# Optimization experiments

Measured on AMD Instinct MI355X. Metric: run time of the kernel, lower is better.

The kernel has to match this reference:

```python
import jax, jax.numpy as jnp
import numpy as np

D_MODEL, HEADS, GROUPS, DIM_HEAD = 256, 8, 8, 64
INNER = HEADS * DIM_HEAD              # 512
OFF_DIMS = INNER // GROUPS            # 64 channels fed to the offset network per group
DF, OFF_SCALE, KS, PAD = 4, 4.0, 6, 1  # downsample_factor, offset_scale, kernel, (6-4)//2
CPB_DIM = D_MODEL // 4                # 64
NUM_LAYERS = 6
SCALE = DIM_HEAD ** -0.5
B, H, W = 1, 40, 40


def grouped_conv1x1(x, w, g):
    # x: (b, cin, h, w); w: (cout, cin//g) torch grouped 1x1 conv weight (squeezed)
    b, cin, h, wd = x.shape
    cout = w.shape[0]
    xg = x.reshape(b, g, cin // g, h, wd)
    wg = w.reshape(g, cout // g, cin // g)
    return jnp.einsum('goi,bgihw->bgohw', wg, xg).reshape(b, cout, h, wd)


def create_grid(h, w, dtype):
    # torch meshgrid(arange(w), arange(h), indexing='xy') stacked at dim 0
    ys, xs = jnp.meshgrid(jnp.arange(h, dtype=dtype), jnp.arange(w, dtype=dtype), indexing='ij')
    return jnp.stack((xs, ys))  # (2, h, w): channel0 = x, channel1 = y


def normalize_grid(grid):
    # faithful to source: channel0 scaled by (h-1), channel1 by (w-1); out dim last
    h, w = grid.shape[-2:]
    g0 = 2.0 * grid[..., 0, :, :] / max(h - 1, 1) - 1.0
    g1 = 2.0 * grid[..., 1, :, :] / max(w - 1, 1) - 1.0
    return jnp.stack((g0, g1), axis=-1)


def grid_sample_bilinear(img, grid):
    # torch F.grid_sample, mode='bilinear', padding_mode='zeros', align_corners=False
    Bn, C, Hh, Ww = img.shape
    gx = ((grid[..., 0] + 1.0) * Ww - 1.0) * 0.5
    gy = ((grid[..., 1] + 1.0) * Hh - 1.0) * 0.5
    x0 = jnp.floor(gx)
    y0 = jnp.floor(gy)
    wx1 = gx - x0
    wy1 = gy - y0
    flat = img.reshape(Bn, C, Hh * Ww)

    def gather(xi, yi):
        valid = (xi >= 0) & (xi <= Ww - 1) & (yi >= 0) & (yi <= Hh - 1)
        xc = jnp.clip(xi, 0, Ww - 1).astype(jnp.int32)
        yc = jnp.clip(yi, 0, Hh - 1).astype(jnp.int32)
        idx = (yc * Ww + xc).reshape(Bn, 1, -1)
        vals = jnp.take_along_axis(flat, idx, axis=2).reshape(Bn, C, *xi.shape[1:])
        return vals * valid[:, None].astype(img.dtype)

    return (gather(x0, y0) * ((1 - wx1) * (1 - wy1))[:, None]
            + gather(x0 + 1, y0) * (wx1 * (1 - wy1))[:, None]
            + gather(x0, y0 + 1) * ((1 - wx1) * wy1)[:, None]
            + gather(x0 + 1, y0 + 1) * (wx1 * wy1)[:, None])


def deform_attn(x, wq, wk, wv, w_off1, b_off1, w_off2,
                cpb_w0, cpb_b0, cpb_w1, cpb_b1, cpb_w2, cpb_b2, w_out, b_out):
    b, c, Hh, Ww = x.shape
    bg = b * GROUPS
    q = grouped_conv1x1(x, wq, GROUPS)                      # (b, 512, H, W)
    qg = q.reshape(bg, OFF_DIMS, Hh, Ww)                    # group heads: (b g) d h w
    # offset network: depthwise 6x6 stride-4 conv -> GELU -> 1x1 -> tanh * scale
    off = jax.lax.conv_general_dilated(
        qg, w_off1, (DF, DF), ((PAD, PAD), (PAD, PAD)),
        dimension_numbers=('NCHW', 'OIHW', 'NCHW'), feature_group_count=OFF_DIMS)
    off = jax.nn.gelu(off + b_off1[None, :, None, None], approximate=False)
    off = jnp.tanh(jnp.einsum('oc,bchw->bohw', w_off2, off)) * OFF_SCALE  # (bg,2,h',w')
    hp, wp = off.shape[-2:]
    vgrid = create_grid(hp, wp, x.dtype)[None] + off
    vgrid_scaled = normalize_grid(vgrid)                    # (bg, h', w', 2)
    xg = x.reshape(bg, c // GROUPS, Hh, Ww)
    kv = grid_sample_bilinear(xg, vgrid_scaled).reshape(b, c, hp, wp)
    k = grouped_conv1x1(kv, wk, GROUPS)
    v = grouped_conv1x1(kv, wv, GROUPS)
    i, j = Hh * Ww, hp * wp
    qh = (q * SCALE).reshape(b, HEADS, DIM_HEAD, i).transpose(0, 1, 3, 2)  # bhid
    kh = k.reshape(b, HEADS, DIM_HEAD, j).transpose(0, 1, 3, 2)
    vh = v.reshape(b, HEADS, DIM_HEAD, j).transpose(0, 1, 3, 2)
    sim = jnp.einsum('bhid,bhjd->bhij', qh, kh)
    # continuous positional bias (CPB, depth-2 MLP on signed-log relative coords)
    grid_q = normalize_grid(create_grid(Hh, Ww, x.dtype)).reshape(i, 2)
    grid_kv = vgrid_scaled.reshape(bg, j, 2)
    pos = grid_q[None, :, None, :] - grid_kv[:, None, :, :]  # (bg, i, j, 2)
    bias = jnp.sign(pos) * jnp.log1p(jnp.abs(pos))
    bias = jax.nn.relu(bias @ cpb_w0.T + cpb_b0)
    bias = jax.nn.relu(bias @ cpb_w1.T + cpb_b1)
    bias = bias @ cpb_w2.T + cpb_b2                          # (bg, i, j, 1)
    sim = sim + bias.reshape(b, GROUPS, i, j)                # heads//offset_groups == 1
    attn = jax.nn.softmax(sim, axis=-1)                      # stable softmax (matches amax-subtract)
    out = jnp.einsum('bhij,bhjd->bhid', attn, vh)
    out = out.transpose(0, 1, 3, 2).reshape(b, INNER, Hh, Ww)
    return jnp.einsum('oc,bchw->bohw', w_out, out) + b_out[None, :, None, None]


def setup_inputs() -> dict:
    key = jax.random.key(0)
    ks = jax.random.split(key, 16)
    L = NUM_LAYERS

    def p(k, shape, scale=0.02):
        return jax.random.normal(k, shape, dtype=jnp.float32) * scale

    return {
        'bev_feat': jax.random.normal(ks[0], (B, D_MODEL, H, W), dtype=jnp.float32),
        'wq': p(ks[1], (L, INNER, D_MODEL // GROUPS)),
        'wk': p(ks[2], (L, INNER, D_MODEL // GROUPS)),
        'wv': p(ks[3], (L, INNER, D_MODEL // GROUPS)),
        'w_off1': p(ks[4], (L, OFF_DIMS, 1, KS, KS)),
        'b_off1': jnp.zeros((L, OFF_DIMS), jnp.float32),
        'w_off2': p(ks[5], (L, 2, OFF_DIMS)),
        'cpb_w0': p(ks[6], (L, CPB_DIM, 2), 0.5),
        'cpb_b0': jnp.zeros((L, CPB_DIM), jnp.float32),
        'cpb_w1': p(ks[7], (L, CPB_DIM, CPB_DIM), 0.1),
        'cpb_b1': jnp.zeros((L, CPB_DIM), jnp.float32),
        'cpb_w2': p(ks[8], (L, 1, CPB_DIM), 0.1),
        'cpb_b2': jnp.zeros((L, 1), jnp.float32),
        'w_out': p(ks[9], (L, D_MODEL, INNER)),
        'b_out': jnp.zeros((L, D_MODEL), jnp.float32),
    }


def reference(bev_feat, wq, wk, wv, w_off1, b_off1, w_off2,
              cpb_w0, cpb_b0, cpb_w1, cpb_b1, cpb_w2, cpb_b2, w_out, b_out):
    # The source encoder loop runs `output = layer(bev_feat)` on the ORIGINAL
    # input each iteration, so only the last layer's output survives. Faithful
    # math = apply layer NUM_LAYERS-1 once (dropout in eval mode -> identity).
    l = NUM_LAYERS - 1
    return deform_attn(bev_feat, wq[l], wk[l], wv[l], w_off1[l], b_off1[l], w_off2[l],
                       cpb_w0[l], cpb_b0[l], cpb_w1[l], cpb_b1[l], cpb_w2[l], cpb_b2[l],
                       w_out[l], b_out[l])
```

## Files before the change

### kernel.cpp

```cpp
#include <hip/hip_runtime.h>
#include <math.h>


#define NP 1600
#define NJ 100

typedef _Float16 f16x8 __attribute__((ext_vector_type(8)));
typedef float  f32x4  __attribute__((ext_vector_type(4)));
typedef float  f32x2  __attribute__((ext_vector_type(2)));

template<int CTRL>
__device__ __forceinline__ float dpp_add(float x) {
  int y = __builtin_amdgcn_update_dpp(0, __builtin_bit_cast(int, x),
                                      CTRL, 0xf, 0xf, true);
  return x + __builtin_bit_cast(float, y);
}

__global__ __launch_bounds__(256) void k_conv1x1(
    const float* __restrict__ x, const float* __restrict__ w,
    float* __restrict__ out, float* __restrict__ out_t) {
  int b = blockIdx.x;
  int g = b / 40;
  int r = b - g * 40;
  int oc = r / 5;
  int p0 = (r - oc * 5) * 320;
  int co0 = g * 64 + oc * 8;
  const float* xg = x + g * 32 * NP;
  const float* wr = w + co0 * 32;
  for (int p = p0 + threadIdx.x; p < p0 + 320; p += 256) {
    float acc[8];
#pragma unroll
    for (int o = 0; o < 8; ++o) acc[o] = 0.f;
#pragma unroll
    for (int ci = 0; ci < 32; ++ci) {
      float xv = xg[ci * NP + p];
#pragma unroll
      for (int o = 0; o < 8; ++o) acc[o] = fmaf(wr[o * 32 + ci], xv, acc[o]);
    }
#pragma unroll
    for (int o = 0; o < 8; ++o) out[(co0 + o) * NP + p] = acc[o];
    f32x4 t0, t1;
    t0[0] = acc[0]; t0[1] = acc[1]; t0[2] = acc[2]; t0[3] = acc[3];
    t1[0] = acc[4]; t1[1] = acc[5]; t1[2] = acc[6]; t1[3] = acc[7];
    *(f32x4*)(out_t + (size_t)p * 512 + co0) = t0;
    *(f32x4*)(out_t + (size_t)p * 512 + co0 + 4) = t1;
  }
}

__global__ __launch_bounds__(256, 4) void k_off_cpb(
    const float* __restrict__ qt, const float* __restrict__ wdw,
    const float* __restrict__ bdw, const float* __restrict__ wo2,
    const float* __restrict__ x, const float* __restrict__ wk,
    const float* __restrict__ wv,
    const float* __restrict__ w0, const float* __restrict__ b0,
    const float* __restrict__ w1, const float* __restrict__ b1v,
    const float* __restrict__ cw2, const float* __restrict__ b2,
    float* __restrict__ kout, float* __restrict__ vout_t,
    float* __restrict__ bias_t) {
  __shared__ float psum[4][72];
  __shared__ float su_l[40];
  __shared__ float sv_l[40];
  __shared__ _Float16 a16[40][72];
  __shared__ _Float16 c16[40][72];
  int gj = blockIdx.x;
  int g = gj / 100;
  int j = gj - g * 100;
  int t = threadIdx.x;
  int lane = t & 63;
  int wv_id = t >> 6;
  int oy = j / 10, ox = j - (j / 10) * 10;

  {
    float acc = 0.f;
    const float* qrow = qt + g * 64 + lane;
#pragma unroll
    for (int tu = 0; tu < 9; ++tu) {
      int tt = wv_id * 9 + tu;
      int ky = tt / 6, kx = tt - (tt / 6) * 6;
      int iy = oy * 4 - 1 + ky;
      int ix = ox * 4 - 1 + kx;
      if (iy >= 0 && iy < 40 && ix >= 0 && ix < 40)
        acc = fmaf(wdw[lane * 36 + tt], qrow[(size_t)(iy * 40 + ix) * 512], acc);
    }
    psum[wv_id][lane] = acc;
  }
  __syncthreads();

  if (wv_id == 0) {
    float accd = psum[0][lane] + psum[1][lane] + psum[2][lane] + psum[3][lane]
               + bdw[lane];
    float od = 0.5f * accd * (1.0f + erff(accd * 0.70710678118654752440f));
    float px = wo2[lane] * od, py = wo2[64 + lane] * od;
#pragma unroll
    for (int m = 1; m < 64; m <<= 1) {
      px += __shfl_xor(px, m);
      py += __shfl_xor(py, m);
    }
    float ax = tanhf(px) * 4.f;
    float ay = tanhf(py) * 4.f;
    float vx = (float)ox + ax;
    float vy = (float)oy + ay;
    float g0 = 2.f * vx / 9.f - 1.f;
    float g1 = 2.f * vy / 9.f - 1.f;
    if (lane < 40) {
      float qc = (float)lane * (2.f / 39.f) - 1.f;
      float u = qc - g0;
      float vv2 = qc - g1;
      su_l[lane] = copysignf(log1pf(fabsf(u)), u);
      sv_l[lane] = copysignf(log1pf(fabsf(vv2)), vv2);
    }
    float gx = ((g0 + 1.f) * 40.f - 1.f) * 0.5f;
    float gy = ((g1 + 1.f) * 40.f - 1.f) * 0.5f;
    float x0f = floorf(gx), y0f = floorf(gy);
    float wx = gx - x0f, wy = gy - y0f;
    bool mx0 = (x0f >= 0.f) && (x0f <= 39.f);
    bool mx1 = (x0f + 1.f >= 0.f) && (x0f + 1.f <= 39.f);
    bool my0 = (y0f >= 0.f) && (y0f <= 39.f);
    bool my1 = (y0f + 1.f >= 0.f) && (y0f + 1.f <= 39.f);
    int ix0 = (int)fminf(fmaxf(x0f, 0.f), 39.f);
    int ix1 = (int)fminf(fmaxf(x0f + 1.f, 0.f), 39.f);
    int iy0 = (int)fminf(fmaxf(y0f, 0.f), 39.f);
    int iy1 = (int)fminf(fmaxf(y0f + 1.f, 0.f), 39.f);
    float w00 = (1.f - wx) * (1.f - wy) * ((mx0 && my0) ? 1.f : 0.f);
    float w10 = wx * (1.f - wy) * ((mx1 && my0) ? 1.f : 0.f);
    float w01 = (1.f - wx) * wy * ((mx0 && my1) ? 1.f : 0.f);
    float w11 = wx * wy * ((mx1 && my1) ? 1.f : 0.f);
    int b00 = iy0 * 40 + ix0, b10 = iy0 * 40 + ix1;
    int b01 = iy1 * 40 + ix0, b11 = iy1 * 40 + ix1;
    float kvc = 0.f;
    if (lane < 32) {
      const float* xc = x + (g * 32 + lane) * NP;
      kvc = w00 * xc[b00] + w10 * xc[b10] + w01 * xc[b01] + w11 * xc[b11];
    }
    const float* wkr = wk + (g * 64 + lane) * 32;
    const float* wvr = wv + (g * 64 + lane) * 32;
    float wkreg[32], wvreg[32];
#pragma unroll
    for (int q4 = 0; q4 < 8; ++q4) {
      f32x4 a = *(const f32x4*)(wkr + q4 * 4);
      f32x4 bq = *(const f32x4*)(wvr + q4 * 4);
#pragma unroll
      for (int e = 0; e < 4; ++e) { wkreg[q4 * 4 + e] = a[e]; wvreg[q4 * 4 + e] = bq[e]; }
    }
    float kacc = 0.f, vacc = 0.f;
#pragma unroll
    for (int c = 0; c < 32; ++c) {
      float kvb = __shfl(kvc, c);
      kacc = fmaf(wkreg[c], kvb, kacc);
      vacc = fmaf(wvreg[c], kvb, vacc);
    }
    kout[(g * 64 + lane) * 100 + j] = kacc;
    vout_t[(size_t)gj * 64 + lane] = vacc;
  }
  __syncthreads();

  for (int idx = t; idx < 2560; idx += 256) {
    int xi = idx >> 6, kk = idx & 63;
    a16[xi][kk] = (_Float16)fmaf(w0[2 * kk], su_l[xi], b0[kk]);
    c16[xi][kk] = (_Float16)(w0[2 * kk + 1] * sv_l[xi]);
  }

  int row = lane & 15;
  int kgrp = lane >> 4;
  f16x8 B[4][2];
#pragma unroll
  for (int ct = 0; ct < 4; ++ct)
#pragma unroll
    for (int s = 0; s < 2; ++s)
#pragma unroll
      for (int e = 0; e < 8; ++e)
        B[ct][s][e] = (_Float16)w1[(ct * 16 + row) * 64 + s * 32 + kgrp * 8 + e];
  float b1c[4], w2c[4];
#pragma unroll
  for (int ct = 0; ct < 4; ++ct) {
    b1c[ct] = b1v[ct * 16 + row];
    w2c[ct] = cw2[ct * 16 + row];
  }
  float bb = b2[0];
  float* outp = bias_t + (size_t)gj * 1600;
  __syncthreads();

  int it0 = wv_id * 25;
  int iy = wv_id * 10;
  int ix = row;
  f16x8 zero8 = {};
  for (int it = it0; it < it0 + 25; ++it) {
    f32x4 acc[4];
#pragma unroll
    for (int ct = 0; ct < 4; ++ct) {
      acc[ct][0] = 0.f; acc[ct][1] = 0.f; acc[ct][2] = 0.f; acc[ct][3] = 0.f;
    }
#pragma unroll
    for (int s = 0; s < 2; ++s) {
      f16x8 av = *(const f16x8*)&a16[ix][s * 32 + kgrp * 8];
      f16x8 cv = *(const f16x8*)&c16[iy][s * 32 + kgrp * 8];
      f16x8 A = __builtin_elementwise_max(av + cv, zero8);
#pragma unroll
      for (int ct = 0; ct < 4; ++ct)
        acc[ct] = __builtin_amdgcn_mfma_f32_16x16x32_f16(A, B[ct][s], acc[ct], 0, 0, 0);
    }
    float part[4];
#pragma unroll
    for (int ri = 0; ri < 4; ++ri) {
      float s2 = 0.f;
#pragma unroll
      for (int ct = 0; ct < 4; ++ct) {
        float val = acc[ct][ri] + b1c[ct];
        s2 = fmaf(w2c[ct], fmaxf(val, 0.f), s2);
      }
      part[ri] = s2;
    }
#pragma unroll
    for (int ri = 0; ri < 4; ++ri) {
      part[ri] = dpp_add<0xB1>(part[ri]);
      part[ri] = dpp_add<0x4E>(part[ri]);
      part[ri] = dpp_add<0x141>(part[ri]);
      part[ri] = dpp_add<0x140>(part[ri]);
    }
    if (row == 0) {
      f32x4 o;
      o[0] = part[0] + bb; o[1] = part[1] + bb;
      o[2] = part[2] + bb; o[3] = part[3] + bb;
      *(f32x4*)(outp + it * 16 + kgrp * 4) = o;
    }
    ix += 16;
    if (ix >= 40) { ix -= 40; ++iy; }
  }
}

__global__ __launch_bounds__(256) void k_attn(
    const float* __restrict__ q, const float* __restrict__ k,
    const float* __restrict__ v_t, const float* __restrict__ bias_t,
    float* __restrict__ inner) {
  __shared__ float v_lds[100][68];
  __shared__ float s_lds[16][100];
  int h = blockIdx.x / 100;
  int i0 = (blockIdx.x - h * 100) * 16;
  int t = threadIdx.x;
  for (int idx = t; idx < 6400; idx += 256) {
    int j = idx >> 6, d = idx & 63;
    v_lds[j][d] = v_t[(size_t)h * 6400 + idx];
  }
  __syncthreads();
  if (t < 200) {
    int ib = (t / 25) * 2, jb = (t % 25) * 4;
    const float* qp = q + h * 64 * NP + i0 + ib;
    const float* kp = k + h * 64 * 100 + jb;
    float a[2][4];
#pragma unroll
    for (int ii = 0; ii < 2; ++ii)
#pragma unroll
      for (int jj = 0; jj < 4; ++jj) a[ii][jj] = 0.f;
#pragma unroll 8
    for (int d = 0; d < 64; ++d) {
      f32x2 qv = *(const f32x2*)(qp + d * NP);
      f32x4 kv4 = *(const f32x4*)(kp + d * 100);
#pragma unroll
      for (int ii = 0; ii < 2; ++ii)
#pragma unroll
        for (int jj = 0; jj < 4; ++jj)
          a[ii][jj] = fmaf(qv[ii], kv4[jj], a[ii][jj]);
    }
    const float* bcol = bias_t + (size_t)h * 100 * 1600;
#pragma unroll
    for (int jj = 0; jj < 4; ++jj) {
      f32x2 bv = *(const f32x2*)(bcol + (size_t)(jb + jj) * 1600 + i0 + ib);
#pragma unroll
      for (int ii = 0; ii < 2; ++ii)
        s_lds[ib + ii][jb + jj] = fmaf(a[ii][jj], 0.125f, bv[ii]);
    }
  }
  __syncthreads();
  {
    int i = t >> 4, sub = t & 15;
    float m = -1e30f;
    for (int j = sub; j < 100; j += 16) m = fmaxf(m, s_lds[i][j]);
#pragma unroll
    for (int off = 1; off < 16; off <<= 1) m = fmaxf(m, __shfl_xor(m, off));
    float sum = 0.f;
    for (int j = sub; j < 100; j += 16) {
      float e = expf(s_lds[i][j] - m);
      s_lds[i][j] = e;
      sum += e;
    }
#pragma unroll
    for (int off = 1; off < 16; off <<= 1) sum += __shfl_xor(sum, off);
    float inv = 1.f / sum;
    for (int j = sub; j < 100; j += 16) s_lds[i][j] *= inv;
  }
  __syncthreads();
  {
    int i = t & 15, db = (t >> 4) * 4;
    float acc[4];
#pragma unroll
    for (int dd = 0; dd < 4; ++dd) acc[dd] = 0.f;
    for (int jc = 0; jc < 25; ++jc) {
      f32x4 sv = *(const f32x4*)&s_lds[i][jc * 4];
#pragma unroll
      for (int jj = 0; jj < 4; ++jj) {
        f32x4 vv = *(const f32x4*)&v_lds[jc * 4 + jj][db];
#pragma unroll
        for (int dd = 0; dd < 4; ++dd)
          acc[dd] = fmaf(sv[jj], vv[dd], acc[dd]);
      }
    }
#pragma unroll
    for (int dd = 0; dd < 4; ++dd)
      inner[(h * 64 + db + dd) * NP + i0 + i] = acc[dd];
  }
}

__global__ __launch_bounds__(256) void k_proj(
    const float* __restrict__ inner, const float* __restrict__ w,
    const float* __restrict__ bo, float* __restrict__ out) {
  int ot = blockIdx.x / 25;
  int pt = blockIdx.x - ot * 25;
  int t = threadIdx.x;
  int quad = __builtin_amdgcn_readfirstlane(t >> 6);
  int o0 = ot * 16 + quad * 4;
  int p = pt * 64 + (t & 63);
  const float* w0r = w + o0 * 512;
  float a0 = 0.f, a1 = 0.f, a2 = 0.f, a3 = 0.f;
#pragma unroll 8
  for (int c = 0; c < 512; ++c) {
    float xv = inner[c * NP + p];
    a0 = fmaf(w0r[c], xv, a0);
    a1 = fmaf(w0r[512 + c], xv, a1);
    a2 = fmaf(w0r[1024 + c], xv, a2);
    a3 = fmaf(w0r[1536 + c], xv, a3);
  }
  out[(o0 + 0) * NP + p] = a0 + bo[o0 + 0];
  out[(o0 + 1) * NP + p] = a1 + bo[o0 + 1];
  out[(o0 + 2) * NP + p] = a2 + bo[o0 + 2];
  out[(o0 + 3) * NP + p] = a3 + bo[o0 + 3];
}

extern "C" void kernel_launch(void* const* d_in, const int* in_sizes, int n_in,
                              void* d_out, int out_size, void* d_ws, size_t ws_size,
                              hipStream_t stream) {
  int L = in_sizes[1] / (512 * 32);
  int l = L - 1;
  const float* x      = (const float*)d_in[0];
  const float* wq     = (const float*)d_in[1]  + (size_t)l * 512 * 32;
  const float* wk     = (const float*)d_in[2]  + (size_t)l * 512 * 32;
  const float* wv     = (const float*)d_in[3]  + (size_t)l * 512 * 32;
  const float* w_off1 = (const float*)d_in[4]  + (size_t)l * 64 * 36;
  const float* b_off1 = (const float*)d_in[5]  + (size_t)l * 64;
  const float* w_off2 = (const float*)d_in[6]  + (size_t)l * 2 * 64;
  const float* cpb_w0 = (const float*)d_in[7]  + (size_t)l * 64 * 2;
  const float* cpb_b0 = (const float*)d_in[8]  + (size_t)l * 64;
  const float* cpb_w1 = (const float*)d_in[9]  + (size_t)l * 64 * 64;
  const float* cpb_b1 = (const float*)d_in[10] + (size_t)l * 64;
  const float* cpb_w2 = (const float*)d_in[11] + (size_t)l * 64;
  const float* cpb_b2 = (const float*)d_in[12] + (size_t)l * 1;
  const float* w_out  = (const float*)d_in[13] + (size_t)l * 256 * 512;
  const float* b_out  = (const float*)d_in[14] + (size_t)l * 256;
  float* out = (float*)d_out;

  float* ws = (float*)d_ws;
  float* q_ws    = ws;
  float* qt_ws   = ws + 819200;
  float* k_ws    = ws + 1638400;
  float* vt_ws   = ws + 1689600;
  float* bias_t  = ws + 1740800;
  float* inner   = ws + 3020800;

  k_conv1x1<<<320, 256, 0, stream>>>(x, wq, q_ws, qt_ws);
  k_off_cpb<<<800, 256, 0, stream>>>(qt_ws, w_off1, b_off1, w_off2, x, wk, wv,
                                     cpb_w0, cpb_b0, cpb_w1, cpb_b1, cpb_w2,
                                     cpb_b2, k_ws, vt_ws, bias_t);
  k_attn<<<800, 256, 0, stream>>>(q_ws, k_ws, vt_ws, bias_t, inner);
  k_proj<<<400, 256, 0, stream>>>(inner, w_out, b_out, out);
}
```

Measured before the change: 102.3 us.

## Fuse four stages into one cooperative persistent kernel with grid syncs

Replaces the four separate launches (q projection, offset/CPB, attention, output projection) with one cooperative kernel of 512 blocks that steps through the stages separated by grid.sync. It also recomputes q inside the attention stage from x and wq instead of reading a stored q buffer. The aim is to remove per-launch overhead and gaps between kernels. In exchange it adds grid-wide barrier cost, leaves some blocks idle in stages with fewer work items, and keeps the old four-kernel path as a fallback if the cooperative launch fails.

Result: slower. 297.9 us (+191.2%).

```diff
diff --git a/kernel.cpp b/kernel.cpp
--- a/kernel.cpp
+++ b/kernel.cpp
@@ -1,5 +1,8 @@
 #include <hip/hip_runtime.h>
+#include <hip/hip_cooperative_groups.h>
 #include <math.h>
+
+namespace cg = cooperative_groups;
 
 
 #define NP 1600
@@ -14,6 +17,332 @@
   int y = __builtin_amdgcn_update_dpp(0, __builtin_bit_cast(int, x),
                                       CTRL, 0xf, 0xf, true);
   return x + __builtin_bit_cast(float, y);
+}
+
+__global__ __launch_bounds__(256, 4) void k_fused(
+    const float* __restrict__ x,   const float* __restrict__ wq,
+    const float* __restrict__ wdw, const float* __restrict__ bdw,
+    const float* __restrict__ wo2,
+    const float* __restrict__ wk,  const float* __restrict__ wvw,
+    const float* __restrict__ w0,  const float* __restrict__ b0,
+    const float* __restrict__ w1,  const float* __restrict__ b1v,
+    const float* __restrict__ cw2, const float* __restrict__ b2,
+    const float* __restrict__ wout, const float* __restrict__ bout,
+    float* __restrict__ qt,  float* __restrict__ kws,
+    float* __restrict__ vt,  float* __restrict__ bias_t,
+    float* __restrict__ inner, float* __restrict__ out) {
+  __shared__ __align__(16) char smem[38720];
+  cg::grid_group grid = cg::this_grid();
+  int b = blockIdx.x;
+  int t = threadIdx.x;
+  int lane = t & 63;
+  int wv_id = t >> 6;
+
+  {
+    int ch = 2 * t;
+    int g = ch >> 6;
+    for (int pp = b; pp < 1600; pp += 512) {
+      float acc0 = 0.f, acc1 = 0.f;
+#pragma unroll
+      for (int ci = 0; ci < 32; ++ci) {
+        float xv = x[(g * 32 + ci) * NP + pp];
+        acc0 = fmaf(wq[(size_t)ch * 32 + ci], xv, acc0);
+        acc1 = fmaf(wq[(size_t)(ch + 1) * 32 + ci], xv, acc1);
+      }
+      f32x2 o; o[0] = acc0; o[1] = acc1;
+      *(f32x2*)(qt + (size_t)pp * 512 + ch) = o;
+    }
+  }
+  grid.sync();
+
+  {
+    float (*psum)[72]   = (float(*)[72])smem;
+    float* su_l         = (float*)(smem + 1152);
+    float* sv_l         = (float*)(smem + 1312);
+    _Float16 (*a16)[72] = (_Float16(*)[72])(smem + 1472);
+    _Float16 (*c16)[72] = (_Float16(*)[72])(smem + 7232);
+    int row = lane & 15;
+    int kgrp = lane >> 4;
+    f16x8 B[4][2];
+#pragma unroll
+    for (int ct = 0; ct < 4; ++ct)
+#pragma unroll
+      for (int s = 0; s < 2; ++s)
+#pragma unroll
+        for (int e = 0; e < 8; ++e)
+          B[ct][s][e] = (_Float16)w1[(ct * 16 + row) * 64 + s * 32 + kgrp * 8 + e];
+    float b1c[4], w2c[4];
+#pragma unroll
+    for (int ct = 0; ct < 4; ++ct) {
+      b1c[ct] = b1v[ct * 16 + row];
+      w2c[ct] = cw2[ct * 16 + row];
+    }
+    float bb = b2[0];
+    f16x8 zero8 = {};
+
+    for (int gj = b; gj < 800; gj += 512) {
+      int g = gj / 100;
+      int j = gj - g * 100;
+      int oy = j / 10, ox = j - (j / 10) * 10;
+
+      {
+        float acc = 0.f;
+        const float* qrow = qt + g * 64 + lane;
+#pragma unroll
+        for (int tu = 0; tu < 9; ++tu) {
+          int tt = wv_id * 9 + tu;
+          int ky = tt / 6, kx = tt - (tt / 6) * 6;
+          int iy = oy * 4 - 1 + ky;
+          int ix = ox * 4 - 1 + kx;
+          if (iy >= 0 && iy < 40 && ix >= 0 && ix < 40)
+            acc = fmaf(wdw[lane * 36 + tt], qrow[(size_t)(iy * 40 + ix) * 512], acc);
+        }
+        psum[wv_id][lane] = acc;
+      }
+      __syncthreads();
+
+      if (wv_id == 0) {
+        float accd = psum[0][lane] + psum[1][lane] + psum[2][lane] + psum[3][lane]
+                   + bdw[lane];
+        float od = 0.5f * accd * (1.0f + erff(accd * 0.70710678118654752440f));
+        float px = wo2[lane] * od, py = wo2[64 + lane] * od;
+#pragma unroll
+        for (int m = 1; m < 64; m <<= 1) {
+          px += __shfl_xor(px, m);
+          py += __shfl_xor(py, m);
+        }
+        float ax = tanhf(px) * 4.f;
+        float ay = tanhf(py) * 4.f;
+        float vx = (float)ox + ax;
+        float vy = (float)oy + ay;
+        float g0 = 2.f * vx / 9.f - 1.f;
+        float g1 = 2.f * vy / 9.f - 1.f;
+        if (lane < 40) {
+          float qc = (float)lane * (2.f / 39.f) - 1.f;
+          float u = qc - g0;
+          float vv2 = qc - g1;
+          su_l[lane] = copysignf(log1pf(fabsf(u)), u);
+          sv_l[lane] = copysignf(log1pf(fabsf(vv2)), vv2);
+        }
+        float gx = ((g0 + 1.f) * 40.f - 1.f) * 0.5f;
+        float gy = ((g1 + 1.f) * 40.f - 1.f) * 0.5f;
+        float x0f = floorf(gx), y0f = floorf(gy);
+        float wx = gx - x0f, wy = gy - y0f;
+        bool mx0 = (x0f >= 0.f) && (x0f <= 39.f);
+        bool mx1 = (x0f + 1.f >= 0.f) && (x0f + 1.f <= 39.f);
+        bool my0 = (y0f >= 0.f) && (y0f <= 39.f);
+        bool my1 = (y0f + 1.f >= 0.f) && (y0f + 1.f <= 39.f);
+        int ix0 = (int)fminf(fmaxf(x0f, 0.f), 39.f);
+        int ix1 = (int)fminf(fmaxf(x0f + 1.f, 0.f), 39.f);
+        int iy0 = (int)fminf(fmaxf(y0f, 0.f), 39.f);
+        int iy1 = (int)fminf(fmaxf(y0f + 1.f, 0.f), 39.f);
+        float w00 = (1.f - wx) * (1.f - wy) * ((mx0 && my0) ? 1.f : 0.f);
+        float w10 = wx * (1.f - wy) * ((mx1 && my0) ? 1.f : 0.f);
+        float w01 = (1.f - wx) * wy * ((mx0 && my1) ? 1.f : 0.f);
+        float w11 = wx * wy * ((mx1 && my1) ? 1.f : 0.f);
+        int b00 = iy0 * 40 + ix0, b10 = iy0 * 40 + ix1;
+        int b01 = iy1 * 40 + ix0, b11 = iy1 * 40 + ix1;
+        float kvc = 0.f;
+        if (lane < 32) {
+          const float* xc = x + (g * 32 + lane) * NP;
+          kvc = w00 * xc[b00] + w10 * xc[b10] + w01 * xc[b01] + w11 * xc[b11];
+        }
+        const float* wkr = wk + (g * 64 + lane) * 32;
+        const float* wvr = wvw + (g * 64 + lane) * 32;
+        float wkreg[32], wvreg[32];
+#pragma unroll
+        for (int q4 = 0; q4 < 8; ++q4) {
+          f32x4 a = *(const f32x4*)(wkr + q4 * 4);
+          f32x4 bq = *(const f32x4*)(wvr + q4 * 4);
+#pragma unroll
+          for (int e = 0; e < 4; ++e) { wkreg[q4 * 4 + e] = a[e]; wvreg[q4 * 4 + e] = bq[e]; }
+        }
+        float kacc = 0.f, vacc = 0.f;
+#pragma unroll
+        for (int c = 0; c < 32; ++c) {
+          float kvb = __shfl(kvc, c);
+          kacc = fmaf(wkreg[c], kvb, kacc);
+          vacc = fmaf(wvreg[c], kvb, vacc);
+        }
+        kws[(g * 64 + lane) * 100 + j] = kacc;
+        vt[(size_t)gj * 64 + lane] = vacc;
+      }
+      __syncthreads();
+
+      for (int idx = t; idx < 2560; idx += 256) {
+        int xi = idx >> 6, kk = idx & 63;
+        a16[xi][kk] = (_Float16)fmaf(w0[2 * kk], su_l[xi], b0[kk]);
+        c16[xi][kk] = (_Float16)(w0[2 * kk + 1] * sv_l[xi]);
+      }
+      __syncthreads();
+
+      float* outp = bias_t + (size_t)gj * 1600;
+      int it0 = wv_id * 25;
+      int iy = wv_id * 10;
+      int ix = row;
+      for (int it = it0; it < it0 + 25; ++it) {
+        f32x4 acc[4];
+#pragma unroll
+        for (int ct = 0; ct < 4; ++ct) {
+          acc[ct][0] = 0.f; acc[ct][1] = 0.f; acc[ct][2] = 0.f; acc[ct][3] = 0.f;
+        }
+#pragma unroll
+        for (int s = 0; s < 2; ++s) {
+          f16x8 av = *(const f16x8*)&a16[ix][s * 32 + kgrp * 8];
+          f16x8 cv = *(const f16x8*)&c16[iy][s * 32 + kgrp * 8];
+          f16x8 A = __builtin_elementwise_max(av + cv, zero8);
+#pragma unroll
+          for (int ct = 0; ct < 4; ++ct)
+            acc[ct] = __builtin_amdgcn_mfma_f32_16x16x32_f16(A, B[ct][s], acc[ct], 0, 0, 0);
+        }
+        float part[4];
+#pragma unroll
+        for (int ri = 0; ri < 4; ++ri) {
+          float s2 = 0.f;
+#pragma unroll
+          for (int ct = 0; ct < 4; ++ct) {
+            float val = acc[ct][ri] + b1c[ct];
+            s2 = fmaf(w2c[ct], fmaxf(val, 0.f), s2);
+          }
+          part[ri] = s2;
+        }
+#pragma unroll
+        for (int ri = 0; ri < 4; ++ri) {
+          part[ri] = dpp_add<0xB1>(part[ri]);
+          part[ri] = dpp_add<0x4E>(part[ri]);
+          part[ri] = dpp_add<0x141>(part[ri]);
+          part[ri] = dpp_add<0x140>(part[ri]);
+        }
+        if (row == 0) {
+          f32x4 o;
+          o[0] = part[0] + bb; o[1] = part[1] + bb;
+          o[2] = part[2] + bb; o[3] = part[3] + bb;
+          *(f32x4*)(outp + it * 16 + kgrp * 4) = o;
+        }
+        ix += 16;
+        if (ix >= 40) { ix -= 40; ++iy; }
+      }
+      __syncthreads();
+    }
+  }
+  grid.sync();
+
+  {
+    float (*v_lds)[68]  = (float(*)[68])smem;
+    float (*s_lds)[100] = (float(*)[100])(smem + 27200);
+    float (*q_lds)[20]  = (float(*)[20])(smem + 33600);
+    for (int u = b; u < 800; u += 512) {
+      int h = u / 100;
+      int i0 = (u - h * 100) * 16;
+      for (int idx = t; idx < 6400; idx += 256) {
+        int j = idx >> 6, d = idx & 63;
+        v_lds[j][d] = vt[(size_t)h * 6400 + idx];
+      }
+      {
+        int d = t & 63;
+        int i4 = t >> 6;
+        f32x4 wr[8];
+#pragma unroll
+        for (int qq = 0; qq < 8; ++qq)
+          wr[qq] = *(const f32x4*)(wq + (size_t)(h * 64 + d) * 32 + qq * 4);
+#pragma unroll
+        for (int ii = 0; ii < 4; ++ii) {
+          int i = i4 * 4 + ii;
+          float acc = 0.f;
+#pragma unroll
+          for (int ci = 0; ci < 32; ++ci)
+            acc = fmaf(wr[ci >> 2][ci & 3], x[(h * 32 + ci) * NP + i0 + i], acc);
+          q_lds[d][i] = acc;
+        }
+      }
+      __syncthreads();
+      if (t < 200) {
+        int ib = (t / 25) * 2, jb = (t % 25) * 4;
+        const float* kp = kws + h * 64 * 100 + jb;
+        float a[2][4];
+#pragma unroll
+        for (int ii = 0; ii < 2; ++ii)
+#pragma unroll
+          for (int jj = 0; jj < 4; ++jj) a[ii][jj] = 0.f;
+#pragma unroll 8
+        for (int d = 0; d < 64; ++d) {
+          f32x2 qv = *(const f32x2*)&q_lds[d][ib];
+          f32x4 kv4 = *(const f32x4*)(kp + d * 100);
+#pragma unroll
+          for (int ii = 0; ii < 2; ++ii)
+#pragma unroll
+            for (int jj = 0; jj < 4; ++jj)
+              a[ii][jj] = fmaf(qv[ii], kv4[jj], a[ii][jj]);
+        }
+        const float* bcol = bias_t + (size_t)h * 100 * 1600;
+#pragma unroll
+        for (int jj = 0; jj < 4; ++jj) {
+          f32x2 bv = *(const f32x2*)(bcol + (size_t)(jb + jj) * 1600 + i0 + ib);
+#pragma unroll
+          for (int ii = 0; ii < 2; ++ii)
+            s_lds[ib + ii][jb + jj] = fmaf(a[ii][jj], 0.125f, bv[ii]);
+        }
+      }
+      __syncthreads();
+      {
+        int i = t >> 4, sub = t & 15;
+        float m = -1e30f;
+        for (int j = sub; j < 100; j += 16) m = fmaxf(m, s_lds[i][j]);
+#pragma unroll
+        for (int off = 1; off < 16; off <<= 1) m = fmaxf(m, __shfl_xor(m, off));
+        float sum = 0.f;
+        for (int j = sub; j < 100; j += 16) {
+          float e = expf(s_lds[i][j] - m);
+          s_lds[i][j] = e;
+          sum += e;
+        }
+#pragma unroll
+        for (int off = 1; off < 16; off <<= 1) sum += __shfl_xor(sum, off);
+        float inv = 1.f / sum;
+        for (int j = sub; j < 100; j += 16) s_lds[i][j] *= inv;
+      }
+      __syncthreads();
+      {
+        int i = t & 15, db = (t >> 4) * 4;
+        float acc[4];
+#pragma unroll
+        for (int dd = 0; dd < 4; ++dd) acc[dd] = 0.f;
+        for (int jc = 0; jc < 25; ++jc) {
+          f32x4 sv = *(const f32x4*)&s_lds[i][jc * 4];
+#pragma unroll
+          for (int jj = 0; jj < 4; ++jj) {
+            f32x4 vv = *(const f32x4*)&v_lds[jc * 4 + jj][db];
+#pragma unroll
+            for (int dd = 0; dd < 4; ++dd)
+              acc[dd] = fmaf(sv[jj], vv[dd], acc[dd]);
+          }
+        }
+#pragma unroll
+        for (int dd = 0; dd < 4; ++dd)
+          inner[(h * 64 + db + dd) * NP + i0 + i] = acc[dd];
+      }
+      __syncthreads();
+    }
+  }
+  grid.sync();
+
+  {
+    for (int u = b; u < 800; u += 512) {
+      int oc = u & 31, pt = u >> 5;
+      int o0 = oc * 8 + (t >> 6) * 2;
+      int p = pt * 64 + (t & 63);
+      const float* w0r = wout + (size_t)o0 * 512;
+      float a0 = 0.f, a1 = 0.f;
+#pragma unroll 8
+      for (int c = 0; c < 512; ++c) {
+        float xv = inner[c * NP + p];
+        a0 = fmaf(w0r[c], xv, a0);
+        a1 = fmaf(w0r[512 + c], xv, a1);
+      }
+      out[(o0 + 0) * NP + p] = a0 + bout[o0 + 0];
+      out[(o0 + 1) * NP + p] = a1 + bout[o0 + 1];
+    }
+  }
 }
 
 __global__ __launch_bounds__(256) void k_conv1x1(
@@ -69,7 +398,6 @@
   int lane = t & 63;
   int wv_id = t >> 6;
   int oy = j / 10, ox = j - (j / 10) * 10;
-
   {
     float acc = 0.f;
     const float* qrow = qt + g * 64 + lane;
@@ -85,7 +413,6 @@
     psum[wv_id][lane] = acc;
   }
   __syncthreads();
-
   if (wv_id == 0) {
     float accd = psum[0][lane] + psum[1][lane] + psum[2][lane] + psum[3][lane]
                + bdw[lane];
@@ -153,13 +480,11 @@
     vout_t[(size_t)gj * 64 + lane] = vacc;
   }
   __syncthreads();
-
   for (int idx = t; idx < 2560; idx += 256) {
     int xi = idx >> 6, kk = idx & 63;
     a16[xi][kk] = (_Float16)fmaf(w0[2 * kk], su_l[xi], b0[kk]);
     c16[xi][kk] = (_Float16)(w0[2 * kk + 1] * sv_l[xi]);
   }
-
   int row = lane & 15;
   int kgrp = lane >> 4;
   f16x8 B[4][2];
@@ -179,7 +504,6 @@
   float bb = b2[0];
   float* outp = bias_t + (size_t)gj * 1600;
   __syncthreads();
-
   int it0 = wv_id * 25;
   int iy = wv_id * 10;
   int ix = row;
@@ -365,10 +689,22 @@
   float* bias_t  = ws + 1740800;
   float* inner   = ws + 3020800;
 
-  k_conv1x1<<<320, 256, 0, stream>>>(x, wq, q_ws, qt_ws);
-  k_off_cpb<<<800, 256, 0, stream>>>(qt_ws, w_off1, b_off1, w_off2, x, wk, wv,
-                                     cpb_w0, cpb_b0, cpb_w1, cpb_b1, cpb_w2,
-                                     cpb_b2, k_ws, vt_ws, bias_t);
-  k_attn<<<800, 256, 0, stream>>>(q_ws, k_ws, vt_ws, bias_t, inner);
-  k_proj<<<400, 256, 0, stream>>>(inner, w_out, b_out, out);
+  void* args[] = {
+    (void*)&x, (void*)&wq, (void*)&w_off1, (void*)&b_off1, (void*)&w_off2,
+    (void*)&wk, (void*)&wv, (void*)&cpb_w0, (void*)&cpb_b0, (void*)&cpb_w1,
+    (void*)&cpb_b1, (void*)&cpb_w2, (void*)&cpb_b2, (void*)&w_out, (void*)&b_out,
+    (void*)&qt_ws, (void*)&k_ws, (void*)&vt_ws, (void*)&bias_t, (void*)&inner,
+    (void*)&out
+  };
+  hipError_t err = hipLaunchCooperativeKernel((void*)k_fused, dim3(512),
+                                              dim3(256), args, 0, stream);
+  if (err != hipSuccess) {
+    (void)hipGetLastError();
+    k_conv1x1<<<320, 256, 0, stream>>>(x, wq, q_ws, qt_ws);
+    k_off_cpb<<<800, 256, 0, stream>>>(qt_ws, w_off1, b_off1, w_off2, x, wk, wv,
+                                       cpb_w0, cpb_b0, cpb_w1, cpb_b1, cpb_w2,
+                                       cpb_b2, k_ws, vt_ws, bias_t);
+    k_attn<<<800, 256, 0, stream>>>(q_ws, k_ws, vt_ws, bias_t, inner);
+    k_proj<<<400, 256, 0, stream>>>(inner, w_out, b_out, out);
+  }
 }
```
